# Kernel optimization log

Hardware: AMD Instinct MI355X
Metric: run time of the kernel (lower is better)

The kernel has to match this reference:

```python
import jax, jax.numpy as jnp
import numpy as np
from jax import lax

# mamba-130m-style config
B, L = 2, 1024          # batch, seq_len
D = 768                 # hidden_size
E = 1536                # intermediate (expand=2)
N = 16                  # ssm state size
R = 48                  # time_step_rank = ceil(D/16)
K = 4                   # conv kernel
NL = 4                  # num layers
NC = 5                  # num classes
EPS = 1e-5


def setup_inputs() -> dict:
    key = jax.random.key(0)
    ks = jax.random.split(key, 10)
    s = 0.02
    return {
        "x": jax.random.normal(ks[0], (B, L, 12), dtype=jnp.float32),
        "proj_w": jax.random.normal(ks[1], (D, 12)) * s,
        "proj_b": jnp.zeros((D,), jnp.float32),
        "norm_w": jnp.ones((NL, D), jnp.float32),
        "in_w": jax.random.normal(ks[2], (NL, 2 * E, D)) * s,
        "conv_w": jax.random.normal(ks[3], (NL, E, K)) * s,
        "conv_b": jnp.zeros((NL, E), jnp.float32),
        "xproj_w": jax.random.normal(ks[4], (NL, R + 2 * N, E)) * s,
        "dt_w": jax.random.normal(ks[5], (NL, E, R)) * s,
        "dt_b": jnp.full((NL, E), -4.0, jnp.float32),  # softplus(-4) ~ small dt
        "A_log": jnp.tile(jnp.log(jnp.arange(1, N + 1, dtype=jnp.float32))[None, None, :], (NL, E, 1)),
        "D_param": jnp.ones((NL, E), jnp.float32),
        "out_w": jax.random.normal(ks[6], (NL, D, E)) * s,
        "fnorm_w": jnp.ones((D,), jnp.float32),
        "cls_w": jax.random.normal(ks[7], (NC, D)) * s,
        "cls_b": jnp.zeros((NC,), jnp.float32),
    }


def _rmsnorm(x, w):
    var = jnp.mean(x * x, axis=-1, keepdims=True)
    return x * lax.rsqrt(var + EPS) * w


def _causal_conv(u, w, b):
    # u: [B,L,E], w: [E,K] depthwise causal conv, left-pad K-1
    up = jnp.pad(u, ((0, 0), (K - 1, 0), (0, 0)))
    y = b
    for k in range(K):
        y = y + w[:, k] * up[:, k:k + L, :]
    return y


def _selective_scan(u, dt, A, Bm, Cm, Dp):
    # u, dt: [B,L,E]; Bm, Cm: [B,L,N]; A: [E,N]; Dp: [E]
    def step(h, inp):
        u_t, dt_t, B_t, C_t = inp  # [B,E],[B,E],[B,N],[B,N]
        dA = jnp.exp(dt_t[:, :, None] * A)                      # [B,E,N]
        h = h * dA + dt_t[:, :, None] * B_t[:, None, :] * u_t[:, :, None]
        y = jnp.einsum('ben,bn->be', h, C_t)
        return h, y

    h0 = jnp.zeros((u.shape[0], E, N), u.dtype)
    _, ys = lax.scan(step, h0,
                     (u.transpose(1, 0, 2), dt.transpose(1, 0, 2),
                      Bm.transpose(1, 0, 2), Cm.transpose(1, 0, 2)))
    return ys.transpose(1, 0, 2) + u * Dp


def reference(x, proj_w, proj_b, norm_w, in_w, conv_w, conv_b, xproj_w,
              dt_w, dt_b, A_log, D_param, out_w, fnorm_w, cls_w, cls_b):
    h = x @ proj_w.T + proj_b                                     # [B,L,D]
    for i in range(NL):
        res = h
        hn = _rmsnorm(h, norm_w[i])
        proj = hn @ in_w[i].T                                     # [B,L,2E]
        u, gate = proj[..., :E], proj[..., E:]
        u = jax.nn.silu(_causal_conv(u, conv_w[i], conv_b[i]))    # [B,L,E]
        xdbc = u @ xproj_w[i].T                                   # [B,L,R+2N]
        dt_r = xdbc[..., :R]
        Bm = xdbc[..., R:R + N]
        Cm = xdbc[..., R + N:]
        dt = jax.nn.softplus(dt_r @ dt_w[i].T + dt_b[i])          # [B,L,E]
        A = -jnp.exp(A_log[i])                                    # [E,N]
        y = _selective_scan(u, dt, A, Bm, Cm, D_param[i])
        y = y * jax.nn.silu(gate)
        h = res + y @ out_w[i].T
    h = _rmsnorm(h, fnorm_w)
    pooled = jnp.mean(h, axis=1)                                  # AdaptiveAvgPool1d(1)
    return pooled @ cls_w.T + cls_b                               # [B,NC]
```

## Files before the change

### kernel.cpp

```cpp
#include <hip/hip_runtime.h>

constexpr int B_  = 2;
constexpr int L_  = 1024;
constexpr int D_  = 768;
constexpr int E_  = 1536;
constexpr int N_  = 16;
constexpr int R_  = 48;
constexpr int NL_ = 4;
constexpr int NC_ = 5;
constexpr int M_  = B_ * L_;
constexpr int E2_ = 2 * E_;
constexpr int XD_ = R_ + 2 * N_;
constexpr float EPS_ = 1e-5f;

constexpr int NCH_ = 16;
constexpr int CL_  = L_ / NCH_;
constexpr int KS_  = 8;
constexpr int PC_  = 8;

typedef __attribute__((ext_vector_type(8))) short bf16x8;
typedef __attribute__((ext_vector_type(4))) float f32x4;
typedef const __attribute__((address_space(1))) void* gas_t;
typedef __attribute__((address_space(3))) void* las_t;

__device__ __forceinline__ float sigm(float x) { return 1.0f / (1.0f + __expf(-x)); }
__device__ __forceinline__ float softplusf(float x) { return x > 20.0f ? x : log1pf(__expf(x)); }
__device__ __forceinline__ ushort f2b(float f) {
  union { float f; unsigned u; } v; v.f = f;
  unsigned r = (v.u + 0x7fffu + ((v.u >> 16) & 1u)) >> 16;
  return (ushort)r;
}
__device__ __forceinline__ float b2f(ushort u) {
  union { unsigned u; float f; } v; v.u = ((unsigned)u) << 16;
  return v.f;
}
__device__ __forceinline__ float b2f_lo(unsigned p) {
  union { unsigned u; float f; } v; v.u = p << 16;
  return v.f;
}
__device__ __forceinline__ float b2f_hi(unsigned p) {
  union { unsigned u; float f; } v; v.u = p & 0xffff0000u;
  return v.f;
}

template <int CTRL>
__device__ __forceinline__ float dpp_add(float x) {
  int yi = __builtin_amdgcn_update_dpp(0, __builtin_bit_cast(int, x), CTRL, 0xf, 0xf, false);
  return x + __builtin_bit_cast(float, yi);
}
__device__ __forceinline__ float row_sum16(float x) {
  x = dpp_add<0x121>(x);
  x = dpp_add<0x122>(x);
  x = dpp_add<0x124>(x);
  x = dpp_add<0x128>(x);
  return x;
}

__device__ __forceinline__ float block_sum(float v, float* sm) {
  #pragma unroll
  for (int o = 32; o > 0; o >>= 1) v += __shfl_xor(v, o);
  if ((threadIdx.x & 63) == 0) sm[threadIdx.x >> 6] = v;
  __syncthreads();
  return sm[0] + sm[1] + sm[2] + sm[3];
}

constexpr int WS1_ = NL_ * E2_ * D_;
constexpr int WS2_ = NL_ * D_ * E_;
constexpr int WS3_ = NL_ * XD_ * E_;
constexpr int WS4_ = NL_ * E_ * 64;
constexpr int WTOT_ = WS1_ + WS2_ + WS3_ + WS4_;
constexpr int WB_ = WTOT_ / 4 / 256;
__global__ __launch_bounds__(256) void k_wprep(const float* __restrict__ in_w, const float* __restrict__ out_w,
                                               const float* __restrict__ xw, const float* __restrict__ dw,
                                               const float* __restrict__ nw,
                                               ushort* __restrict__ in_wb, ushort* __restrict__ out_wb,
                                               ushort* __restrict__ xwb, ushort* __restrict__ dtwb,
                                               const float* __restrict__ x, const float* __restrict__ pw,
                                               const float* __restrict__ pb, float* __restrict__ h,
                                               ushort* __restrict__ hb) {
  if (blockIdx.x >= WB_) {
    __shared__ float xs[12];
    int bx = blockIdx.x - WB_;
    int m = bx / 3;
    int d = (bx % 3) * 256 + threadIdx.x;
    if (threadIdx.x < 12) xs[threadIdx.x] = x[m * 12 + threadIdx.x];
    __syncthreads();
    float acc = pb[d];
    #pragma unroll
    for (int j = 0; j < 12; j++) acc = fmaf(xs[j], pw[d * 12 + j], acc);
    h[(size_t)m * D_ + d] = acc;
    hb[(size_t)m * D_ + d] = f2b(acc);
    return;
  }
  int i = (blockIdx.x * 256 + threadIdx.x) * 4;
  if (i < WS1_) {
    float4 v = *(const float4*)(in_w + i);
    int l = i / (E2_ * D_);
    int d = i % D_;
    float4 w = *(const float4*)(nw + l * D_ + d);
    *(ushort4*)(in_wb + i) = make_ushort4(f2b(v.x * w.x), f2b(v.y * w.y), f2b(v.z * w.z), f2b(v.w * w.w));
  } else if (i < WS1_ + WS2_) {
    int j = i - WS1_;
    float4 v = *(const float4*)(out_w + j);
    *(ushort4*)(out_wb + j) = make_ushort4(f2b(v.x), f2b(v.y), f2b(v.z), f2b(v.w));
  } else if (i < WS1_ + WS2_ + WS3_) {
    int j = i - WS1_ - WS2_;
    float4 v = *(const float4*)(xw + j);
    *(ushort4*)(xwb + j) = make_ushort4(f2b(v.x), f2b(v.y), f2b(v.z), f2b(v.w));
  } else {
    int j = i - WS1_ - WS2_ - WS3_;
    int k = j & 63, e = j >> 6;
    ushort4 o;
    o.x = (k + 0 < R_) ? f2b(dw[e * R_ + k + 0]) : (ushort)0;
    o.y = (k + 1 < R_) ? f2b(dw[e * R_ + k + 1]) : (ushort)0;
    o.z = (k + 2 < R_) ? f2b(dw[e * R_ + k + 2]) : (ushort)0;
    o.w = (k + 3 < R_) ? f2b(dw[e * R_ + k + 3]) : (ushort)0;
    *(ushort4*)(dtwb + j) = o;
  }
}

__global__ __launch_bounds__(256) void k_sumsq(const float* __restrict__ h, float* __restrict__ ssq) {
  __shared__ float sm[4];
  int m = blockIdx.x, tid = threadIdx.x;
  const float* row = h + (size_t)m * D_;
  float v0 = row[tid], v1 = row[tid + 256], v2 = row[tid + 512];
  float s = block_sum(v0 * v0 + v1 * v1 + v2 * v2, sm);
  if (tid == 0) ssq[m] = s;
}

template <int BM, int BN, int MODE>
__global__ __launch_bounds__(256) void k_gemm_bf(const ushort* __restrict__ A, const ushort* __restrict__ Bw,
                                                 void* __restrict__ Cv, const float* __restrict__ res,
                                                 ushort* __restrict__ Cb, float* __restrict__ ssq,
                                                 int Kd, int Nd) {
  constexpr int AM = BM / 32, BNF = BN / 32;
  __shared__ ushort sA[BM * 32];
  __shared__ ushort sB[BN * 32];
  const int tid = threadIdx.x;
  const int wave = tid >> 6, lane = tid & 63;
  const int q = lane >> 4, r = lane & 15;
  const int wm = wave >> 1, wn = wave & 1;
  const int m0 = blockIdx.y * BM, n0 = blockIdx.x * BN;
  f32x4 acc[AM][BNF] = {};

  for (int k0 = 0; k0 < Kd; k0 += 32) {
    #pragma unroll
    for (int j = 0; j < BM / 64; j++) {
      int i = j * 256 + tid;
      const ushort* gp = A + (size_t)(m0 + (i >> 2)) * Kd + k0 + ((i & 3) << 3);
      __builtin_amdgcn_global_load_lds((gas_t)gp, (las_t)(sA + ((j * 256 + wave * 64) << 3)), 16, 0, 0);
    }
    #pragma unroll
    for (int j = 0; j < BN / 64; j++) {
      int i = j * 256 + tid;
      const ushort* gp = Bw + (size_t)(n0 + (i >> 2)) * Kd + k0 + ((i & 3) << 3);
      __builtin_amdgcn_global_load_lds((gas_t)gp, (las_t)(sB + ((j * 256 + wave * 64) << 3)), 16, 0, 0);
    }
    __syncthreads();
    bf16x8 af[AM], bfv[BNF];
    #pragma unroll
    for (int mi = 0; mi < AM; mi++)
      af[mi] = *(const bf16x8*)&sA[(wm * (BM / 2) + mi * 16 + r) * 32 + q * 8];
    #pragma unroll
    for (int nj = 0; nj < BNF; nj++)
      bfv[nj] = *(const bf16x8*)&sB[(wn * (BN / 2) + nj * 16 + r) * 32 + q * 8];
    #pragma unroll
    for (int mi = 0; mi < AM; mi++)
      #pragma unroll
      for (int nj = 0; nj < BNF; nj++)
        acc[mi][nj] = __builtin_amdgcn_mfma_f32_16x16x32_bf16(af[mi], bfv[nj], acc[mi][nj], 0, 0, 0);
    __syncthreads();
  }
  #pragma unroll
  for (int mi = 0; mi < AM; mi++) {
    #pragma unroll
    for (int rg = 0; rg < 4; rg++) {
      int row = m0 + wm * (BM / 2) + mi * 16 + q * 4 + rg;
      float rs = 0.0f, ssl = 0.0f;
      if (MODE == 4) rs = rsqrtf(res[row] * (1.0f / D_) + EPS_);
      #pragma unroll
      for (int nj = 0; nj < BNF; nj++) {
        int col = n0 + wn * (BN / 2) + nj * 16 + r;
        size_t off = (size_t)row * Nd + col;
        float v = acc[mi][nj][rg];
        if (MODE == 3) {
          ((ushort*)Cv)[off] = f2b(v);
        } else if (MODE == 4) {
          ((ushort*)Cv)[off] = f2b(v * rs);
        } else if (MODE == 5) {
          v += res[off];
          ((float*)Cv)[off] = v;
          Cb[off] = f2b(v);
          ssl = fmaf(v, v, ssl);
        } else {
          if (MODE == 1) v += res[off];
          if (MODE == 2) v = softplusf(v + res[col]);
          ((float*)Cv)[off] = v;
        }
      }
      if (MODE == 5) {
        float sr = row_sum16(ssl);
        if (r == 0) atomicAdd(&ssq[row], sr);
      }
    }
  }
}

__global__ __launch_bounds__(256) void k_gemm_x(const ushort* __restrict__ A, const ushort* __restrict__ Bw,
                                                float* __restrict__ part) {
  __shared__ ushort sA[64 * 32];
  __shared__ ushort sB[80 * 32];
  const int tid = threadIdx.x;
  const int wave = tid >> 6, lane = tid & 63;
  const int q = lane >> 4, r = lane & 15;
  const int m0 = blockIdx.x * 64;
  const int kbeg = blockIdx.y * (E_ / KS_), kend = kbeg + E_ / KS_;
  f32x4 acc[5] = {};

  for (int k0 = kbeg; k0 < kend; k0 += 32) {
    {
      const ushort* gp = A + (size_t)(m0 + wave * 16 + (lane >> 2)) * E_ + k0 + ((lane & 3) << 3);
      __builtin_amdgcn_global_load_lds((gas_t)gp, (las_t)(sA + (wave << 9)), 16, 0, 0);
    }
    #pragma unroll
    for (int j = wave; j < 5; j += 4) {
      const ushort* gp = Bw + (size_t)(j * 16 + (lane >> 2)) * E_ + k0 + ((lane & 3) << 3);
      __builtin_amdgcn_global_load_lds((gas_t)gp, (las_t)(sB + (j << 9)), 16, 0, 0);
    }
    __syncthreads();
    bf16x8 af = *(const bf16x8*)&sA[(wave * 16 + r) * 32 + q * 8];
    #pragma unroll
    for (int nj = 0; nj < 5; nj++) {
      bf16x8 bfv = *(const bf16x8*)&sB[(nj * 16 + r) * 32 + q * 8];
      acc[nj] = __builtin_amdgcn_mfma_f32_16x16x32_bf16(af, bfv, acc[nj], 0, 0, 0);
    }
    __syncthreads();
  }
  float* pp = part + (size_t)blockIdx.y * M_ * XD_;
  #pragma unroll
  for (int nj = 0; nj < 5; nj++) {
    int col = nj * 16 + r;
    #pragma unroll
    for (int rg = 0; rg < 4; rg++) {
      int row = m0 + wave * 16 + q * 4 + rg;
      pp[(size_t)row * XD_ + col] = acc[nj][rg];
    }
  }
}

__global__ __launch_bounds__(256) void k_xfin(const float* __restrict__ part, float* __restrict__ xdbc,
                                              ushort* __restrict__ xb, float* __restrict__ ssq) {
  int i = blockIdx.x * 256 + threadIdx.x;
  if (i < M_) ssq[i] = 0.0f;
  int m = i / XD_, col = i - m * XD_;
  float s = 0.0f;
  #pragma unroll
  for (int ks = 0; ks < KS_; ks++) s += part[(size_t)ks * M_ * XD_ + i];
  xdbc[i] = s;
  if (col < R_) xb[(size_t)m * 64 + col] = f2b(s);
  else if (col < 64) xb[(size_t)m * 64 + col] = 0;
}

constexpr int TC_ = 4;
__global__ __launch_bounds__(384) void k_conv2(const ushort* __restrict__ proj, const float* __restrict__ cw,
                                               const float* __restrict__ cb, ushort* __restrict__ ub16,
                                               ushort* __restrict__ gb16) {
  int m0 = blockIdx.x * TC_;
  int t0 = m0 & (L_ - 1);
  int base = m0 - t0;
  int e4 = threadIdx.x * 4;
  float wv[4][4];
  #pragma unroll
  for (int j = 0; j < 4; j++) {
    float4 w = *(const float4*)(cw + (e4 + j) * 4);
    wv[j][0] = w.x; wv[j][1] = w.y; wv[j][2] = w.z; wv[j][3] = w.w;
  }
  float4 bb = *(const float4*)(cb + e4);
  float bbv[4] = {bb.x, bb.y, bb.z, bb.w};
  float win[4][4];
  #pragma unroll
  for (int s = 0; s < 3; s++) {
    int t = t0 - 3 + s;
    if (t >= 0) {
      uint2 p = *(const uint2*)(proj + (size_t)(base + t) * E2_ + e4);
      win[s][0] = b2f_lo(p.x); win[s][1] = b2f_hi(p.x);
      win[s][2] = b2f_lo(p.y); win[s][3] = b2f_hi(p.y);
    } else {
      win[s][0] = win[s][1] = win[s][2] = win[s][3] = 0.0f;
    }
  }
  #pragma unroll
  for (int j = 0; j < TC_; j++) {
    size_t m = (size_t)(m0 + j);
    uint2 p = *(const uint2*)(proj + m * E2_ + e4);
    win[3][0] = b2f_lo(p.x); win[3][1] = b2f_hi(p.x);
    win[3][2] = b2f_lo(p.y); win[3][3] = b2f_hi(p.y);
    float o[4];
    #pragma unroll
    for (int c = 0; c < 4; c++) {
      float a = bbv[c];
      a = fmaf(wv[c][0], win[0][c], a);
      a = fmaf(wv[c][1], win[1][c], a);
      a = fmaf(wv[c][2], win[2][c], a);
      a = fmaf(wv[c][3], win[3][c], a);
      o[c] = a * sigm(a);
    }
    uint2 uo;
    uo.x = (unsigned)f2b(o[0]) | ((unsigned)f2b(o[1]) << 16);
    uo.y = (unsigned)f2b(o[2]) | ((unsigned)f2b(o[3]) << 16);
    *(uint2*)(ub16 + m * E_ + e4) = uo;
    #pragma unroll
    for (int s = 0; s < 3; s++) {
      win[s][0] = win[s + 1][0]; win[s][1] = win[s + 1][1];
      win[s][2] = win[s + 1][2]; win[s][3] = win[s + 1][3];
    }
  }
  #pragma unroll
  for (int j = 0; j < TC_; j++) {
    size_t m = (size_t)(m0 + j);
    uint2 g = *(const uint2*)(proj + m * E2_ + E_ + e4);
    float g0 = b2f_lo(g.x), g1 = b2f_hi(g.x), g2 = b2f_lo(g.y), g3 = b2f_hi(g.y);
    g0 *= sigm(g0); g1 *= sigm(g1); g2 *= sigm(g2); g3 *= sigm(g3);
    uint2 go;
    go.x = (unsigned)f2b(g0) | ((unsigned)f2b(g1) << 16);
    go.y = (unsigned)f2b(g2) | ((unsigned)f2b(g3) << 16);
    *(uint2*)(gb16 + m * E_ + e4) = go;
  }
}

__global__ __launch_bounds__(256, 6) void k_scanA(const ushort* __restrict__ u, const float* __restrict__ dtb,
                                                  const float* __restrict__ xdbc, const float* __restrict__ A_log,
                                                  float* __restrict__ Pst, float* __restrict__ Sst) {
  __shared__ float2 s_dtu[CL_][16];
  __shared__ float  s_b [CL_][16];
  const int tid = threadIdx.x;
  const int e0 = blockIdx.x << 4;
  const int b  = blockIdx.y;
  const int c  = blockIdx.z;
  const int n  = tid & 15, el = tid >> 4;
  const int e  = e0 + el;
  const float A = -__expf(A_log[e * N_ + n]);
  const int t0 = c * CL_;

  float r_dt[4], r_b[4];
  ushort r_u[4];
  #pragma unroll
  for (int j = 0; j < 4; j++) {
    size_t m = (size_t)(b * L_ + t0 + j * 16 + el);
    r_dt[j] = dtb[m * E_ + e0 + n];
    r_u[j]  = u[m * E_ + e0 + n];
    int idx = j * 256 + tid;
    r_b[j] = xdbc[(size_t)(b * L_ + t0 + (idx >> 4)) * XD_ + R_ + (idx & 15)];
  }
  #pragma unroll
  for (int j = 0; j < 4; j++) {
    int t = j * 16 + el;
    s_dtu[t][n] = make_float2(r_dt[j], r_dt[j] * b2f(r_u[j]));
    int idx = j * 256 + tid;
    s_b[idx >> 4][idx & 15] = r_b[j];
  }
  __syncthreads();

  float hs = 0.0f, pp = 1.0f;
  #pragma unroll 8
  for (int t = 0; t < CL_; t++) {
    float2 dtu = s_dtu[t][el];
    float dA = __expf(dtu.x * A);
    hs = fmaf(hs, dA, dtu.y * s_b[t][n]);
    pp *= dA;
  }
  size_t o = (((size_t)(b * NCH_ + c) * E_) + e) * N_ + n;
  Pst[o] = pp;
  Sst[o] = hs;
}

__global__ __launch_bounds__(256, 6) void k_scanC(const ushort* __restrict__ u, const float* __restrict__ dtb,
                                                  const float* __restrict__ xdbc, const ushort* __restrict__ gb,
                                                  const float* __restrict__ A_log, const float* __restrict__ Dp,
                                                  const float* __restrict__ Pst, const float* __restrict__ Sst,
                                                  ushort* __restrict__ y) {
  __shared__ float2 s_dtu[CL_][16];
  __shared__ float2 s_bc [CL_][16];
  __shared__ float2 s_og [CL_][16];
  __shared__ ushort s_y [CL_][16];
  const int tid = threadIdx.x;
  const int e0 = blockIdx.x << 4;
  const int b  = blockIdx.y;
  const int c  = blockIdx.z;
  const int n  = tid & 15, el = tid >> 4;
  const int e  = e0 + el;
  const float A = -__expf(A_log[e * N_ + n]);
  const float Dv = Dp[e0 + n];
  const int t0 = c * CL_;

  float r_dt[4], r_bc[8];
  ushort r_u[4], r_g[4];
  #pragma unroll
  for (int j = 0; j < 4; j++) {
    size_t m = (size_t)(b * L_ + t0 + j * 16 + el);
    r_dt[j] = dtb[m * E_ + e0 + n];
    r_u[j]  = u[m * E_ + e0 + n];
    r_g[j]  = gb[m * E_ + e0 + n];
  }
  #pragma unroll
  for (int j = 0; j < 8; j++) {
    int idx = j * 256 + tid;
    r_bc[j] = xdbc[(size_t)(b * L_ + t0 + (idx >> 5)) * XD_ + R_ + (idx & 31)];
  }

  float hs = 0.0f;
  if (c > 0) {
    float pv[NCH_ - 1], sv[NCH_ - 1];
    #pragma unroll
    for (int cc = 0; cc < NCH_ - 1; cc++) {
      int ci = cc < c ? cc : c - 1;
      size_t o = (((size_t)(b * NCH_ + ci) * E_) + e) * N_ + n;
      pv[cc] = Pst[o];
      sv[cc] = Sst[o];
    }
    #pragma unroll
    for (int cc = 0; cc < NCH_ - 1; cc++) {
      bool v = cc < c;
      hs = fmaf(v ? pv[cc] : 1.0f, hs, v ? sv[cc] : 0.0f);
    }
  }

  #pragma unroll
  for (int j = 0; j < 4; j++) {
    int t = j * 16 + el;
    float uf = b2f(r_u[j]);
    s_dtu[t][n] = make_float2(r_dt[j], r_dt[j] * uf);
    s_og[t][n] = make_float2(uf * Dv, b2f(r_g[j]));
  }
  #pragma unroll
  for (int j = 0; j < 8; j++) {
    int idx = j * 256 + tid;
    int t = idx >> 5, col = idx & 31;
    ((float*)&s_bc[t][0])[((col & 15) << 1) + (col >> 4)] = r_bc[j];
  }
  __syncthreads();

  #pragma unroll 8
  for (int t = 0; t < CL_; t++) {
    float2 dtu = s_dtu[t][el];
    float2 bc  = s_bc[t][n];
    float dA = __expf(dtu.x * A);
    hs = fmaf(hs, dA, dtu.y * bc.x);
    float p = row_sum16(hs * bc.y);
    if (n == 0) {
      float2 og = s_og[t][el];
      s_y[t][el] = f2b((p + og.x) * og.y);
    }
  }
  __syncthreads();

  {
    int row = tid >> 2, seg = tid & 3;
    uint2 v = *(const uint2*)&s_y[row][seg * 4];
    *(uint2*)(y + (size_t)(b * L_ + t0 + row) * E_ + e0 + seg * 4) = v;
  }
}

__global__ __launch_bounds__(256) void k_rowscale(const float* __restrict__ h, float* __restrict__ rs) {
  __shared__ float sm[4];
  int m = blockIdx.x, tid = threadIdx.x;
  const float* row = h + (size_t)m * D_;
  float v0 = row[tid], v1 = row[tid + 256], v2 = row[tid + 512];
  float s = block_sum(v0 * v0 + v1 * v1 + v2 * v2, sm);
  if (tid == 0) rs[m] = rsqrtf(s * (1.0f / D_) + EPS_);
}

__global__ __launch_bounds__(256) void k_pool(const float* __restrict__ h, const float* __restrict__ rs,
                                              float* __restrict__ pooledP) {
  int d = blockIdx.x * 256 + threadIdx.x;
  int pc = blockIdx.y;
  int b = blockIdx.z;
  int t0 = pc * (L_ / PC_);
  float acc = 0.0f;
  for (int t = t0; t < t0 + L_ / PC_; t++) {
    int m = b * L_ + t;
    acc = fmaf(h[(size_t)m * D_ + d], rs[m], acc);
  }
  pooledP[((size_t)pc * B_ + b) * D_ + d] = acc;
}

__global__ __launch_bounds__(256) void k_logits(const float* __restrict__ pooledP, const float* __restrict__ fw,
                                                const float* __restrict__ cw, const float* __restrict__ cb,
                                                float* __restrict__ out) {
  __shared__ float sp[B_ * D_];
  int tid = threadIdx.x;
  for (int d = tid; d < B_ * D_; d += 256) {
    int b = d / D_, dd = d - b * D_;
    float pd = 0.0f;
    #pragma unroll
    for (int pc = 0; pc < PC_; pc++) pd += pooledP[((size_t)pc * B_ + b) * D_ + dd];
    sp[d] = pd * fw[dd] * (1.0f / L_);
  }
  __syncthreads();
  int wv = tid >> 6, ln = tid & 63;
  for (int p = wv; p < B_ * NC_; p += 4) {
    int b = p / NC_, c = p % NC_;
    float s = 0.0f;
    for (int d = ln; d < D_; d += 64) s = fmaf(sp[b * D_ + d], cw[c * D_ + d], s);
    #pragma unroll
    for (int o = 32; o > 0; o >>= 1) s += __shfl_xor(s, o);
    if (ln == 0) out[p] = s + cb[c];
  }
}

extern "C" void kernel_launch(void* const* d_in, const int* in_sizes, int n_in,
                              void* d_out, int out_size, void* d_ws, size_t ws_size,
                              hipStream_t stream) {
  const float* x       = (const float*)d_in[0];
  const float* proj_w  = (const float*)d_in[1];
  const float* proj_b  = (const float*)d_in[2];
  const float* norm_w  = (const float*)d_in[3];
  const float* in_w    = (const float*)d_in[4];
  const float* conv_w  = (const float*)d_in[5];
  const float* conv_b  = (const float*)d_in[6];
  const float* xproj_w = (const float*)d_in[7];
  const float* dt_w    = (const float*)d_in[8];
  const float* dt_b    = (const float*)d_in[9];
  const float* A_log   = (const float*)d_in[10];
  const float* D_param = (const float*)d_in[11];
  const float* out_w   = (const float*)d_in[12];
  const float* fnorm_w = (const float*)d_in[13];
  const float* cls_w   = (const float*)d_in[14];
  const float* cls_b   = (const float*)d_in[15];
  float* out = (float*)d_out;

  float* h      = (float*)d_ws;
  float* xdbc   = h + (size_t)M_ * D_;
  float* dtbuf  = xdbc + (size_t)M_ * XD_;
  float* rsb    = dtbuf + (size_t)M_ * E_;
  float* ssq    = rsb + M_;
  float* pooledP = ssq + M_;
  float* Pst    = pooledP + (size_t)PC_ * B_ * D_;
  float* Sst    = Pst + (size_t)B_ * NCH_ * E_ * N_;
  float* xpart  = Sst + (size_t)B_ * NCH_ * E_ * N_;
  ushort* proj_bf = (ushort*)(xpart + (size_t)KS_ * M_ * XD_);
  ushort* hb_bf   = proj_bf + (size_t)M_ * E2_;
  ushort* y_bf    = hb_bf + (size_t)M_ * D_;
  ushort* ub_bf   = y_bf + (size_t)M_ * E_;
  ushort* g_bf    = ub_bf + (size_t)M_ * E_;
  ushort* xdbc_bf = g_bf + (size_t)M_ * E_;
  ushort* xwb     = xdbc_bf + (size_t)M_ * 64;
  ushort* dtwb    = xwb + (size_t)NL_ * XD_ * E_;
  ushort* in_wb   = dtwb + (size_t)NL_ * E_ * 64;
  ushort* out_wb  = in_wb + (size_t)NL_ * E2_ * D_;

  k_wprep<<<WB_ + 3 * M_, 256, 0, stream>>>(in_w, out_w, xproj_w, dt_w, norm_w,
                                            in_wb, out_wb, xwb, dtwb,
                                            x, proj_w, proj_b, h, hb_bf);
  k_sumsq<<<M_, 256, 0, stream>>>(h, ssq);

  for (int i = 0; i < NL_; i++) {
    k_gemm_bf<128, 128, 4><<<dim3(E2_ / 128, M_ / 128), 256, 0, stream>>>(
        hb_bf, in_wb + (size_t)i * E2_ * D_, proj_bf, ssq, nullptr, nullptr, D_, E2_);
    k_conv2<<<M_ / TC_, 384, 0, stream>>>(proj_bf, conv_w + i * E_ * 4, conv_b + i * E_, ub_bf, g_bf);
    k_gemm_x<<<dim3(M_ / 64, KS_), 256, 0, stream>>>(ub_bf, xwb + (size_t)i * XD_ * E_, xpart);
    k_xfin<<<M_ * XD_ / 256, 256, 0, stream>>>(xpart, xdbc, xdbc_bf, ssq);
    k_gemm_bf<64, 64, 2><<<dim3(E_ / 64, M_ / 64), 256, 0, stream>>>(
        xdbc_bf, dtwb + (size_t)i * E_ * 64, dtbuf, dt_b + i * E_, nullptr, nullptr, 64, E_);
    k_scanA<<<dim3(E_ / 16, B_, NCH_), 256, 0, stream>>>(ub_bf, dtbuf, xdbc,
                                                         A_log + (size_t)i * E_ * N_, Pst, Sst);
    k_scanC<<<dim3(E_ / 16, B_, NCH_), 256, 0, stream>>>(ub_bf, dtbuf, xdbc, g_bf,
                                                         A_log + (size_t)i * E_ * N_, D_param + i * E_,
                                                         Pst, Sst, y_bf);
    k_gemm_bf<64, 64, 5><<<dim3(D_ / 64, M_ / 64), 256, 0, stream>>>(
        y_bf, out_wb + (size_t)i * D_ * E_, h, h, hb_bf, ssq, E_, D_);
  }

  k_rowscale<<<M_, 256, 0, stream>>>(h, rsb);
  k_pool<<<dim3(D_ / 256, PC_, B_), 256, 0, stream>>>(h, rsb, pooledP);
  k_logits<<<1, 256, 0, stream>>>(pooledP, fnorm_w, cls_w, cls_b, out);
}
```

Before: 669.8 us.

## Fuse dt projection into scan kernels and fold norm/pool reductions

Drops the separate dt GEMM and its fp32 [M,E] buffer. Both scan kernels now compute dt for their chunk with a small MFMA over the 64-wide xdbc_bf row and apply softplus in-kernel, which removes a large global write and two reads per layer at the cost of doing the dt GEMM twice. The initial sum-of-squares kernel is folded into the input projection via atomics after a memset. The final rowscale kernel is merged into a pooling kernel with more partial chunks. Risks include duplicated MFMA work, extra launch-time memset, and serialized per-row block reductions in pooling.

```diff
diff --git a/kernel.cpp b/kernel.cpp
--- a/kernel.cpp
+++ b/kernel.cpp
@@ -16,7 +16,7 @@
 constexpr int NCH_ = 16;
 constexpr int CL_  = L_ / NCH_;
 constexpr int KS_  = 8;
-constexpr int PC_  = 8;
+constexpr int PC_  = 64;
 
 typedef __attribute__((ext_vector_type(8))) short bf16x8;
 typedef __attribute__((ext_vector_type(4))) float f32x4;
@@ -77,9 +77,10 @@
                                                ushort* __restrict__ xwb, ushort* __restrict__ dtwb,
                                                const float* __restrict__ x, const float* __restrict__ pw,
                                                const float* __restrict__ pb, float* __restrict__ h,
-                                               ushort* __restrict__ hb) {
+                                               ushort* __restrict__ hb, float* __restrict__ ssq) {
   if (blockIdx.x >= WB_) {
     __shared__ float xs[12];
+    __shared__ float sm[4];
     int bx = blockIdx.x - WB_;
     int m = bx / 3;
     int d = (bx % 3) * 256 + threadIdx.x;
@@ -90,6 +91,8 @@
     for (int j = 0; j < 12; j++) acc = fmaf(xs[j], pw[d * 12 + j], acc);
     h[(size_t)m * D_ + d] = acc;
     hb[(size_t)m * D_ + d] = f2b(acc);
+    float s = block_sum(acc * acc, sm);
+    if (threadIdx.x == 0) atomicAdd(&ssq[m], s);
     return;
   }
   int i = (blockIdx.x * 256 + threadIdx.x) * 4;
@@ -119,15 +122,6 @@
   }
 }
 
-__global__ __launch_bounds__(256) void k_sumsq(const float* __restrict__ h, float* __restrict__ ssq) {
-  __shared__ float sm[4];
-  int m = blockIdx.x, tid = threadIdx.x;
-  const float* row = h + (size_t)m * D_;
-  float v0 = row[tid], v1 = row[tid + 256], v2 = row[tid + 512];
-  float s = block_sum(v0 * v0 + v1 * v1 + v2 * v2, sm);
-  if (tid == 0) ssq[m] = s;
-}
-
 template <int BM, int BN, int MODE>
 __global__ __launch_bounds__(256) void k_gemm_bf(const ushort* __restrict__ A, const ushort* __restrict__ Bw,
                                                  void* __restrict__ Cv, const float* __restrict__ res,
@@ -183,19 +177,13 @@
         int col = n0 + wn * (BN / 2) + nj * 16 + r;
         size_t off = (size_t)row * Nd + col;
         float v = acc[mi][nj][rg];
-        if (MODE == 3) {
-          ((ushort*)Cv)[off] = f2b(v);
-        } else if (MODE == 4) {
+        if (MODE == 4) {
           ((ushort*)Cv)[off] = f2b(v * rs);
         } else if (MODE == 5) {
           v += res[off];
           ((float*)Cv)[off] = v;
           Cb[off] = f2b(v);
           ssl = fmaf(v, v, ssl);
-        } else {
-          if (MODE == 1) v += res[off];
-          if (MODE == 2) v = softplusf(v + res[col]);
-          ((float*)Cv)[off] = v;
         }
       }
       if (MODE == 5) {
@@ -328,45 +316,54 @@
   }
 }
 
-__global__ __launch_bounds__(256, 6) void k_scanA(const ushort* __restrict__ u, const float* __restrict__ dtb,
+__global__ __launch_bounds__(256, 6) void k_scanA(const ushort* __restrict__ u, const ushort* __restrict__ xb,
+                                                  const ushort* __restrict__ dtw, const float* __restrict__ dtb_p,
                                                   const float* __restrict__ xdbc, const float* __restrict__ A_log,
                                                   float* __restrict__ Pst, float* __restrict__ Sst) {
-  __shared__ float2 s_dtu[CL_][16];
-  __shared__ float  s_b [CL_][16];
+  __shared__ float s_dt[CL_][16];
+  __shared__ float s_u [CL_][16];
+  __shared__ float s_b [CL_][16];
   const int tid = threadIdx.x;
   const int e0 = blockIdx.x << 4;
   const int b  = blockIdx.y;
   const int c  = blockIdx.z;
   const int n  = tid & 15, el = tid >> 4;
   const int e  = e0 + el;
+  const int wave = tid >> 6, lane = tid & 63;
+  const int q = lane >> 4, r = lane & 15;
   const float A = -__expf(A_log[e * N_ + n]);
   const int t0 = c * CL_;
-
-  float r_dt[4], r_b[4];
-  ushort r_u[4];
-  #pragma unroll
-  for (int j = 0; j < 4; j++) {
-    size_t m = (size_t)(b * L_ + t0 + j * 16 + el);
-    r_dt[j] = dtb[m * E_ + e0 + n];
-    r_u[j]  = u[m * E_ + e0 + n];
-    int idx = j * 256 + tid;
-    r_b[j] = xdbc[(size_t)(b * L_ + t0 + (idx >> 4)) * XD_ + R_ + (idx & 15)];
-  }
+  const int mb = b * L_ + t0;
+
+  f32x4 dacc = {};
+  #pragma unroll
+  for (int k0 = 0; k0 < 64; k0 += 32) {
+    bf16x8 af = *(const bf16x8*)&xb[(size_t)(mb + wave * 16 + r) * 64 + k0 + q * 8];
+    bf16x8 bfv = *(const bf16x8*)&dtw[(e0 + r) * 64 + k0 + q * 8];
+    dacc = __builtin_amdgcn_mfma_f32_16x16x32_bf16(af, bfv, dacc, 0, 0, 0);
+  }
+  {
+    float db = dtb_p[e0 + r];
+    #pragma unroll
+    for (int rg = 0; rg < 4; rg++)
+      s_dt[wave * 16 + q * 4 + rg][r] = softplusf(dacc[rg] + db);
+  }
+
   #pragma unroll
   for (int j = 0; j < 4; j++) {
     int t = j * 16 + el;
-    s_dtu[t][n] = make_float2(r_dt[j], r_dt[j] * b2f(r_u[j]));
+    s_u[t][n] = b2f(u[(size_t)(mb + t) * E_ + e0 + n]);
     int idx = j * 256 + tid;
-    s_b[idx >> 4][idx & 15] = r_b[j];
+    s_b[idx >> 4][idx & 15] = xdbc[(size_t)(mb + (idx >> 4)) * XD_ + R_ + (idx & 15)];
   }
   __syncthreads();
 
   float hs = 0.0f, pp = 1.0f;
   #pragma unroll 8
   for (int t = 0; t < CL_; t++) {
-    float2 dtu = s_dtu[t][el];
-    float dA = __expf(dtu.x * A);
-    hs = fmaf(hs, dA, dtu.y * s_b[t][n]);
+    float dtv = s_dt[t][el];
+    float dA = __expf(dtv * A);
+    hs = fmaf(hs, dA, dtv * s_u[t][el] * s_b[t][n]);
     pp *= dA;
   }
   size_t o = (((size_t)(b * NCH_ + c) * E_) + e) * N_ + n;
@@ -374,14 +371,16 @@
   Sst[o] = hs;
 }
 
-__global__ __launch_bounds__(256, 6) void k_scanC(const ushort* __restrict__ u, const float* __restrict__ dtb,
+__global__ __launch_bounds__(256, 6) void k_scanC(const ushort* __restrict__ u, const ushort* __restrict__ xb,
+                                                  const ushort* __restrict__ dtw, const float* __restrict__ dtb_p,
                                                   const float* __restrict__ xdbc, const ushort* __restrict__ gb,
                                                   const float* __restrict__ A_log, const float* __restrict__ Dp,
                                                   const float* __restrict__ Pst, const float* __restrict__ Sst,
                                                   ushort* __restrict__ y) {
-  __shared__ float2 s_dtu[CL_][16];
-  __shared__ float2 s_bc [CL_][16];
-  __shared__ float2 s_og [CL_][16];
+  __shared__ float  s_dt[CL_][16];
+  __shared__ float  s_u [CL_][16];
+  __shared__ float2 s_bc[CL_][16];
+  __shared__ float2 s_og[CL_][16];
   __shared__ ushort s_y [CL_][16];
   const int tid = threadIdx.x;
   const int e0 = blockIdx.x << 4;
@@ -389,23 +388,32 @@
   const int c  = blockIdx.z;
   const int n  = tid & 15, el = tid >> 4;
   const int e  = e0 + el;
+  const int wave = tid >> 6, lane = tid & 63;
+  const int q = lane >> 4, r = lane & 15;
   const float A = -__expf(A_log[e * N_ + n]);
   const float Dv = Dp[e0 + n];
   const int t0 = c * CL_;
-
-  float r_dt[4], r_bc[8];
-  ushort r_u[4], r_g[4];
-  #pragma unroll
-  for (int j = 0; j < 4; j++) {
-    size_t m = (size_t)(b * L_ + t0 + j * 16 + el);
-    r_dt[j] = dtb[m * E_ + e0 + n];
-    r_u[j]  = u[m * E_ + e0 + n];
-    r_g[j]  = gb[m * E_ + e0 + n];
-  }
+  const int mb = b * L_ + t0;
+
+  f32x4 dacc = {};
+  #pragma unroll
+  for (int k0 = 0; k0 < 64; k0 += 32) {
+    bf16x8 af = *(const bf16x8*)&xb[(size_t)(mb + wave * 16 + r) * 64 + k0 + q * 8];
+    bf16x8 bfv = *(const bf16x8*)&dtw[(e0 + r) * 64 + k0 + q * 8];
+    dacc = __builtin_amdgcn_mfma_f32_16x16x32_bf16(af, bfv, dacc, 0, 0, 0);
+  }
+  {
+    float db = dtb_p[e0 + r];
+    #pragma unroll
+    for (int rg = 0; rg < 4; rg++)
+      s_dt[wave * 16 + q * 4 + rg][r] = softplusf(dacc[rg] + db);
+  }
+
+  float r_bc[8];
   #pragma unroll
   for (int j = 0; j < 8; j++) {
     int idx = j * 256 + tid;
-    r_bc[j] = xdbc[(size_t)(b * L_ + t0 + (idx >> 5)) * XD_ + R_ + (idx & 31)];
+    r_bc[j] = xdbc[(size_t)(mb + (idx >> 5)) * XD_ + R_ + (idx & 31)];
   }
 
   float hs = 0.0f;
@@ -428,9 +436,9 @@
   #pragma unroll
   for (int j = 0; j < 4; j++) {
     int t = j * 16 + el;
-    float uf = b2f(r_u[j]);
-    s_dtu[t][n] = make_float2(r_dt[j], r_dt[j] * uf);
-    s_og[t][n] = make_float2(uf * Dv, b2f(r_g[j]));
+    float uf = b2f(u[(size_t)(mb + t) * E_ + e0 + n]);
+    s_u[t][n] = uf;
+    s_og[t][n] = make_float2(uf * Dv, b2f(gb[(size_t)(mb + t) * E_ + e0 + n]));
   }
   #pragma unroll
   for (int j = 0; j < 8; j++) {
@@ -442,10 +450,10 @@
 
   #pragma unroll 8
   for (int t = 0; t < CL_; t++) {
-    float2 dtu = s_dtu[t][el];
+    float dtv = s_dt[t][el];
     float2 bc  = s_bc[t][n];
-    float dA = __expf(dtu.x * A);
-    hs = fmaf(hs, dA, dtu.y * bc.x);
+    float dA = __expf(dtv * A);
+    hs = fmaf(hs, dA, dtv * s_u[t][el] * bc.x);
     float p = row_sum16(hs * bc.y);
     if (n == 0) {
       float2 og = s_og[t][el];
@@ -457,31 +465,26 @@
   {
     int row = tid >> 2, seg = tid & 3;
     uint2 v = *(const uint2*)&s_y[row][seg * 4];
-    *(uint2*)(y + (size_t)(b * L_ + t0 + row) * E_ + e0 + seg * 4) = v;
-  }
-}
-
-__global__ __launch_bounds__(256) void k_rowscale(const float* __restrict__ h, float* __restrict__ rs) {
+    *(uint2*)(y + (size_t)(mb + row) * E_ + e0 + seg * 4) = v;
+  }
+}
+
+__global__ __launch_bounds__(256) void k_pool(const float* __restrict__ h, float* __restrict__ pooledP) {
   __shared__ float sm[4];
-  int m = blockIdx.x, tid = threadIdx.x;
-  const float* row = h + (size_t)m * D_;
-  float v0 = row[tid], v1 = row[tid + 256], v2 = row[tid + 512];
-  float s = block_sum(v0 * v0 + v1 * v1 + v2 * v2, sm);
-  if (tid == 0) rs[m] = rsqrtf(s * (1.0f / D_) + EPS_);
-}
-
-__global__ __launch_bounds__(256) void k_pool(const float* __restrict__ h, const float* __restrict__ rs,
-                                              float* __restrict__ pooledP) {
-  int d = blockIdx.x * 256 + threadIdx.x;
-  int pc = blockIdx.y;
-  int b = blockIdx.z;
-  int t0 = pc * (L_ / PC_);
-  float acc = 0.0f;
-  for (int t = t0; t < t0 + L_ / PC_; t++) {
-    int m = b * L_ + t;
-    acc = fmaf(h[(size_t)m * D_ + d], rs[m], acc);
-  }
-  pooledP[((size_t)pc * B_ + b) * D_ + d] = acc;
+  const int pc = blockIdx.x, b = blockIdx.y;
+  const int tid = threadIdx.x;
+  const int t0 = pc * (L_ / PC_);
+  float a0 = 0.0f, a1 = 0.0f, a2 = 0.0f;
+  for (int rowi = 0; rowi < L_ / PC_; rowi++) {
+    const float* hr = h + (size_t)(b * L_ + t0 + rowi) * D_;
+    float v0 = hr[tid], v1 = hr[tid + 256], v2 = hr[tid + 512];
+    float s = block_sum(v0 * v0 + v1 * v1 + v2 * v2, sm);
+    float rs = rsqrtf(s * (1.0f / D_) + EPS_);
+    a0 = fmaf(v0, rs, a0); a1 = fmaf(v1, rs, a1); a2 = fmaf(v2, rs, a2);
+    __syncthreads();
+  }
+  float* pp = pooledP + ((size_t)pc * B_ + b) * D_;
+  pp[tid] = a0; pp[tid + 256] = a1; pp[tid + 512] = a2;
 }
 
 __global__ __launch_bounds__(256) void k_logits(const float* __restrict__ pooledP, const float* __restrict__ fw,
@@ -492,7 +495,7 @@
   for (int d = tid; d < B_ * D_; d += 256) {
     int b = d / D_, dd = d - b * D_;
     float pd = 0.0f;
-    #pragma unroll
+    #pragma unroll 8
     for (int pc = 0; pc < PC_; pc++) pd += pooledP[((size_t)pc * B_ + b) * D_ + dd];
     sp[d] = pd * fw[dd] * (1.0f / L_);
   }
@@ -531,9 +534,7 @@
 
   float* h      = (float*)d_ws;
   float* xdbc   = h + (size_t)M_ * D_;
-  float* dtbuf  = xdbc + (size_t)M_ * XD_;
-  float* rsb    = dtbuf + (size_t)M_ * E_;
-  float* ssq    = rsb + M_;
+  float* ssq    = xdbc + (size_t)M_ * XD_;
   float* pooledP = ssq + M_;
   float* Pst    = pooledP + (size_t)PC_ * B_ * D_;
   float* Sst    = Pst + (size_t)B_ * NCH_ * E_ * N_;
@@ -549,29 +550,28 @@
   ushort* in_wb   = dtwb + (size_t)NL_ * E_ * 64;
   ushort* out_wb  = in_wb + (size_t)NL_ * E2_ * D_;
 
+  hipMemsetAsync(ssq, 0, M_ * sizeof(float), stream);
   k_wprep<<<WB_ + 3 * M_, 256, 0, stream>>>(in_w, out_w, xproj_w, dt_w, norm_w,
                                             in_wb, out_wb, xwb, dtwb,
-                                            x, proj_w, proj_b, h, hb_bf);
-  k_sumsq<<<M_, 256, 0, stream>>>(h, ssq);
+                                            x, proj_w, proj_b, h, hb_bf, ssq);
 
   for (int i = 0; i < NL_; i++) {
     k_gemm_bf<128, 128, 4><<<dim3(E2_ / 128, M_ / 128), 256, 0, stream>>>(
         hb_bf, in_wb + (size_t)i * E2_ * D_, proj_bf, ssq, nullptr, nullptr, D_, E2_);
-    k_conv2<<<M_ / TC_, 384, 0, stream>>>(proj_bf, conv_w + i * E_ * 4, conv_b + i * E_, ub_bf, g_bf);
+    k_conv2<<<M_ / TC_, 384, 0, stream>>>(proj_bf, conv_w + i * E_ * 4, conv_b + i * E_,
+                                          ub_bf, g_bf);
     k_gemm_x<<<dim3(M_ / 64, KS_), 256, 0, stream>>>(ub_bf, xwb + (size_t)i * XD_ * E_, xpart);
     k_xfin<<<M_ * XD_ / 256, 256, 0, stream>>>(xpart, xdbc, xdbc_bf, ssq);
-    k_gemm_bf<64, 64, 2><<<dim3(E_ / 64, M_ / 64), 256, 0, stream>>>(
-        xdbc_bf, dtwb + (size_t)i * E_ * 64, dtbuf, dt_b + i * E_, nullptr, nullptr, 64, E_);
-    k_scanA<<<dim3(E_ / 16, B_, NCH_), 256, 0, stream>>>(ub_bf, dtbuf, xdbc,
-                                                         A_log + (size_t)i * E_ * N_, Pst, Sst);
-    k_scanC<<<dim3(E_ / 16, B_, NCH_), 256, 0, stream>>>(ub_bf, dtbuf, xdbc, g_bf,
-                                                         A_log + (size_t)i * E_ * N_, D_param + i * E_,
-                                                         Pst, Sst, y_bf);
+    k_scanA<<<dim3(E_ / 16, B_, NCH_), 256, 0, stream>>>(
+        ub_bf, xdbc_bf, dtwb + (size_t)i * E_ * 64, dt_b + (size_t)i * E_, xdbc,
+        A_log + (size_t)i * E_ * N_, Pst, Sst);
+    k_scanC<<<dim3(E_ / 16, B_, NCH_), 256, 0, stream>>>(
+        ub_bf, xdbc_bf, dtwb + (size_t)i * E_ * 64, dt_b + (size_t)i * E_, xdbc, g_bf,
+        A_log + (size_t)i * E_ * N_, D_param + i * E_, Pst, Sst, y_bf);
     k_gemm_bf<64, 64, 5><<<dim3(D_ / 64, M_ / 64), 256, 0, stream>>>(
         y_bf, out_wb + (size_t)i * D_ * E_, h, h, hb_bf, ssq, E_, D_);
   }
 
-  k_rowscale<<<M_, 256, 0, stream>>>(h, rsb);
-  k_pool<<<dim3(D_ / 256, PC_, B_), 256, 0, stream>>>(h, rsb, pooledP);
+  k_pool<<<dim3(PC_, B_), 256, 0, stream>>>(h, pooledP);
   k_logits<<<1, 256, 0, stream>>>(pooledP, fnorm_w, cls_w, cls_b, out);
 }
```

New measurement: 679.6 us. About the same (+1.5%).
